# Kernel optimization log

Hardware: AMD Instinct MI355X
Metric: run time of the kernel (lower is better)

## Reference

```python
import jax, jax.numpy as jnp
import numpy as np

OCC_W, SMOOTH_W, SPARSE_W, CONS_W = 1.0, 0.1, 0.01, 0.1
EPS = 1e-7  # torch BCE clamps log terms; clip preds for numerical parity


def setup_inputs() -> dict:
    key = jax.random.key(0)
    k1, k2, k3, k4 = jax.random.split(key, 4)
    N, F = 16384, 64
    predictions = jax.random.uniform(k1, (N,), dtype=jnp.float32, minval=1e-4, maxval=1.0 - 1e-4)
    targets = jax.random.uniform(k2, (N,), dtype=jnp.float32)
    features = jax.random.normal(k3, (N, F), dtype=jnp.float32)
    points = jax.random.normal(k4, (N, 3), dtype=jnp.float32)
    return {"predictions": predictions, "targets": targets, "features": features, "points": points}


def reference(predictions, targets, features, points):
    # --- occupancy loss: BCE(mean) ---
    p = jnp.clip(predictions, EPS, 1.0 - EPS)
    occupancy = -jnp.mean(targets * jnp.log(p) + (1.0 - targets) * jnp.log1p(-p))

    # --- smoothness loss: for each point, 3 nearest neighbors (excl. self) ---
    # Fused all-pairs sq-distance [N, N] + top-k, replacing the per-point python loop.
    sq = jnp.sum(points * points, axis=1)                      # [N]
    d2 = sq[:, None] + sq[None, :] - 2.0 * (points @ points.T)  # [N, N]
    d2 = jnp.maximum(d2, 0.0)  # monotone in distance, so ordering == torch.norm ordering
    _, idx = jax.lax.top_k(-d2, 4)                              # 4 smallest distances
    nn_idx = idx[:, 1:4]                                        # drop self (index 0)
    # per-point local gradient: mean |pred_i - pred_nn|, then mean over points
    smoothness = jnp.mean(jnp.abs(predictions[:, None] - predictions[nn_idx]))

    # --- sparsity loss: mean |features| ---
    sparsity = jnp.mean(jnp.abs(features))

    # --- consistency loss: MSE ---
    consistency = jnp.mean((predictions - targets) ** 2)

    total = (OCC_W * occupancy + SMOOTH_W * smoothness
             + SPARSE_W * sparsity + CONS_W * consistency)
    return total
```

## Files before the change

### kernel.cpp

```cpp
#include <hip/hip_runtime.h>
#include <float.h>
#include <math.h>


constexpr int   N_ = 16384;
constexpr int   F_ = 64;
constexpr float OCC_W = 1.0f, SMOOTH_W = 0.1f, SPARSE_W = 0.01f, CONS_W = 0.1f;
constexpr float EPS_ = 1e-7f;

__device__ __forceinline__ void ins4f(float t, float& b0, float& b1, float& b2, float& b3) {
  float n0 = fminf(b0, t);
  float n1 = __builtin_amdgcn_fmed3f(b0, b1, t);
  float n2 = __builtin_amdgcn_fmed3f(b1, b2, t);
  float n3 = __builtin_amdgcn_fmed3f(b2, b3, t);
  b0 = n0; b1 = n1; b2 = n2; b3 = n3;
}


template <int CHUNKS>
__global__ __launch_bounds__(256) void knn_kernel(const float* __restrict__ pts,
                                                  float4* __restrict__ cand,
                                                  unsigned* __restrict__ done) {
  constexpr int CHUNK   = N_ / CHUNKS;
  constexpr int TILE    = CHUNK;
  constexpr int NOCT    = TILE / 8;
  constexpr int ITEMS   = 4;
  constexpr int IPG     = 1024;
  constexpr int IGROUPS = N_ / IPG;
  if (blockIdx.x == 0 && threadIdx.x == 0) *done = 0u;

  int igrp  = blockIdx.x % IGROUPS;
  int chunk = blockIdx.x / IGROUPS;
  int j0    = chunk * CHUNK;

  __shared__ float4 Q[TILE];
  for (int t = threadIdx.x; t < TILE; t += 256) {
    int j = j0 + t;
    float x = pts[3 * j], y = pts[3 * j + 1], z = pts[3 * j + 2];
    Q[t] = make_float4(-2.f * x, -2.f * y, -2.f * z, fmaf(x, x, fmaf(y, y, z * z)));
  }

  float xi[ITEMS], yi[ITEMS], zi[ITEMS];
  float b0[ITEMS], b1[ITEMS], b2[ITEMS], b3[ITEMS];
#pragma unroll
  for (int k = 0; k < ITEMS; ++k) {
    int i = igrp * IPG + threadIdx.x + k * 256;
    xi[k] = pts[3 * i]; yi[k] = pts[3 * i + 1]; zi[k] = pts[3 * i + 2];
    b0[k] = b1[k] = b2[k] = b3[k] = FLT_MAX;
  }
  __syncthreads();

  unsigned obase = (unsigned)(j0 >> 3);

  float4 c0 = Q[0], c1 = Q[1], c2 = Q[2], c3 = Q[3],
         c4 = Q[4], c5 = Q[5], c6 = Q[6], c7 = Q[7];
  for (int oct = 0; oct < NOCT; ++oct) {
    int nb = ((oct + 1) & (NOCT - 1)) * 8;
    float4 n0 = Q[nb + 0], n1 = Q[nb + 1], n2 = Q[nb + 2], n3 = Q[nb + 3],
           n4 = Q[nb + 4], n5 = Q[nb + 5], n6 = Q[nb + 6], n7 = Q[nb + 7];
    unsigned ok = obase + (unsigned)oct;
#pragma unroll
    for (int k = 0; k < ITEMS; ++k) {
      float x = xi[k], y = yi[k], z = zi[k];
      float t0 = fmaf(x, c0.x, fmaf(y, c0.y, fmaf(z, c0.z, c0.w)));
      float t1 = fmaf(x, c1.x, fmaf(y, c1.y, fmaf(z, c1.z, c1.w)));
      float t2 = fmaf(x, c2.x, fmaf(y, c2.y, fmaf(z, c2.z, c2.w)));
      float t3 = fmaf(x, c3.x, fmaf(y, c3.y, fmaf(z, c3.z, c3.w)));
      float t4 = fmaf(x, c4.x, fmaf(y, c4.y, fmaf(z, c4.z, c4.w)));
      float t5 = fmaf(x, c5.x, fmaf(y, c5.y, fmaf(z, c5.z, c5.w)));
      float t6 = fmaf(x, c6.x, fmaf(y, c6.y, fmaf(z, c6.z, c6.w)));
      float t7 = fmaf(x, c7.x, fmaf(y, c7.y, fmaf(z, c7.z, c7.w)));
      float m = fminf(fminf(fminf(t0, t1), fminf(t2, t3)),
                      fminf(fminf(t4, t5), fminf(t6, t7)));
      float kf = __uint_as_float((__float_as_uint(m) & 0xFFFFF000u) | ok);
      ins4f(kf, b0[k], b1[k], b2[k], b3[k]);
    }
    c0 = n0; c1 = n1; c2 = n2; c3 = n3; c4 = n4; c5 = n5; c6 = n6; c7 = n7;
  }

#pragma unroll
  for (int k = 0; k < ITEMS; ++k) {
    int i = igrp * IPG + threadIdx.x + k * 256;
    cand[(size_t)chunk * N_ + i] = make_float4(b0[k], b1[k], b2[k], b3[k]);
  }
}

template <int CHUNKS>
__global__ __launch_bounds__(256) void merge_kernel(const float* __restrict__ pred,
                                                    const float* __restrict__ targ,
                                                    const float* __restrict__ feat,
                                                    const float* __restrict__ pts,
                                                    const float4* __restrict__ cand,
                                                    float4* __restrict__ part,
                                                    unsigned* __restrict__ done,
                                                    float* __restrict__ out) {
  __shared__ float4 sh[256];
  __shared__ float ws4[4][4];
  __shared__ int is_last;
  constexpr int CPT = CHUNKS / 4;
  int tid  = threadIdx.x;
  int lane = tid & 63;
  int sub  = tid >> 6;
  int i = blockIdx.x * 64 + lane;

  const float4* f4 = (const float4*)feat;
  float s_sp = 0.f;
#pragma unroll
  for (int s = 0; s < 4; ++s) {
    float4 v = f4[(size_t)s * 65536 + blockIdx.x * 256 + tid];
    s_sp += fabsf(v.x) + fabsf(v.y) + fabsf(v.z) + fabsf(v.w);
  }

  float b0 = FLT_MAX, b1 = FLT_MAX, b2 = FLT_MAX, b3 = FLT_MAX;
#pragma unroll 4
  for (int cc = 0; cc < CPT; ++cc) {
    float4 v = cand[(size_t)(sub * CPT + cc) * N_ + i];
    ins4f(v.x, b0, b1, b2, b3);
    ins4f(v.y, b0, b1, b2, b3);
    ins4f(v.z, b0, b1, b2, b3);
    ins4f(v.w, b0, b1, b2, b3);
  }
  sh[tid] = make_float4(b0, b1, b2, b3);
  __syncthreads();

  float s_occ = 0.f, s_cons = 0.f, s_sm = 0.f;
  if (sub == 0) {
#pragma unroll
    for (int w = 1; w < 4; ++w) {
      float4 v = sh[w * 64 + lane];
      ins4f(v.x, b0, b1, b2, b3);
      ins4f(v.y, b0, b1, b2, b3);
      ins4f(v.z, b0, b1, b2, b3);
      ins4f(v.w, b0, b1, b2, b3);
    }
    unsigned qarr[4] = {__float_as_uint(b0) & 0xFFFu, __float_as_uint(b1) & 0xFFFu,
                        __float_as_uint(b2) & 0xFFFu, __float_as_uint(b3) & 0xFFFu};
    float xi = pts[3 * i], yi = pts[3 * i + 1], zi = pts[3 * i + 2];
    float c0 = FLT_MAX, c1 = FLT_MAX, c2 = FLT_MAX;
    float p0 = 0.f, p1 = 0.f, p2 = 0.f;
#pragma unroll
    for (int s = 0; s < 4; ++s) {
#pragma unroll
      for (int m = 0; m < 8; ++m) {
        int j = (int)(qarr[s] * 8 + m);
        float dx = xi - pts[3 * j], dy = yi - pts[3 * j + 1], dz = zi - pts[3 * j + 2];
        float d2 = fmaf(dx, dx, fmaf(dy, dy, dz * dz));
        float pj = pred[j];
        if (j != i && d2 < c2) {
          bool cc0 = d2 < c0, cc1 = d2 < c1;
          float n2 = cc1 ? c1 : d2;               float m2 = cc1 ? p1 : pj;
          float n1 = cc0 ? c0 : (cc1 ? d2 : c1);  float m1 = cc0 ? p0 : (cc1 ? pj : p1);
          float n0 = cc0 ? d2 : c0;               float m0 = cc0 ? pj : p0;
          c0 = n0; c1 = n1; c2 = n2; p0 = m0; p1 = m1; p2 = m2;
        }
      }
    }
    float pi = pred[i], tg = targ[i];
    float p  = fminf(fmaxf(pi, EPS_), 1.0f - EPS_);
    s_occ  = -(tg * __logf(p) + (1.0f - tg) * __logf(1.0f - p));
    float dd = pi - tg;
    s_cons = dd * dd;
    s_sm   = fabsf(pi - p0) + fabsf(pi - p1) + fabsf(pi - p2);
  }

  for (int off = 32; off > 0; off >>= 1) {
    s_sp   += __shfl_down(s_sp, off);
    s_occ  += __shfl_down(s_occ, off);
    s_cons += __shfl_down(s_cons, off);
    s_sm   += __shfl_down(s_sm, off);
  }
  if ((tid & 63) == 0) {
    int w = tid >> 6;
    ws4[w][0] = s_occ; ws4[w][1] = s_cons; ws4[w][2] = s_sp; ws4[w][3] = s_sm;
  }
  __syncthreads();
  if (tid == 0) {
    part[blockIdx.x] = make_float4(ws4[0][0] + ws4[1][0] + ws4[2][0] + ws4[3][0],
                                   ws4[0][1] + ws4[1][1] + ws4[2][1] + ws4[3][1],
                                   ws4[0][2] + ws4[1][2] + ws4[2][2] + ws4[3][2],
                                   ws4[0][3] + ws4[1][3] + ws4[2][3] + ws4[3][3]);
    __threadfence();
    unsigned prev = atomicAdd(done, 1u);
    is_last = (prev == (unsigned)(gridDim.x - 1));
  }
  __syncthreads();

  if (is_last) {
    __threadfence();
    float4 a = part[tid];
    float o = a.x, cn = a.y, sp = a.z, sm = a.w;
    for (int off = 32; off > 0; off >>= 1) {
      o  += __shfl_down(o, off);
      cn += __shfl_down(cn, off);
      sp += __shfl_down(sp, off);
      sm += __shfl_down(sm, off);
    }
    if ((tid & 63) == 0) {
      int w = tid >> 6;
      ws4[w][0] = o; ws4[w][1] = cn; ws4[w][2] = sp; ws4[w][3] = sm;
    }
    __syncthreads();
    if (tid == 0) {
      float occ  = ws4[0][0] + ws4[1][0] + ws4[2][0] + ws4[3][0];
      float cons = ws4[0][1] + ws4[1][1] + ws4[2][1] + ws4[3][1];
      float spar = ws4[0][2] + ws4[1][2] + ws4[2][2] + ws4[3][2];
      float smoo = ws4[0][3] + ws4[1][3] + ws4[2][3] + ws4[3][3];
      out[0] = OCC_W * (occ / (float)N_)
             + CONS_W * (cons / (float)N_)
             + SPARSE_W * (spar / (float)(N_ * F_))
             + SMOOTH_W * (smoo / (float)(N_ * 3));
    }
  }
}

extern "C" void kernel_launch(void* const* d_in, const int* in_sizes, int n_in,
                              void* d_out, int out_size, void* d_ws, size_t ws_size,
                              hipStream_t stream) {
  const float* pred = (const float*)d_in[0];
  const float* targ = (const float*)d_in[1];
  const float* feat = (const float*)d_in[2];
  const float* pts  = (const float*)d_in[3];
  float* out = (float*)d_out;

  char*     ws   = (char*)d_ws;
  float4*   part = (float4*)ws;
  unsigned* done = (unsigned*)(ws + 4096);
  float4*   cand = (float4*)(ws + 8192);

  size_t base = 8192;
  auto need = [&](int c) { return base + (size_t)c * N_ * 16; };
  if (ws_size >= need(64)) {
    knn_kernel<64><<<16 * 64, 256, 0, stream>>>(pts, cand, done);
    merge_kernel<64><<<256, 256, 0, stream>>>(pred, targ, feat, pts, cand, part, done, out);
  } else if (ws_size >= need(32)) {
    knn_kernel<32><<<16 * 32, 256, 0, stream>>>(pts, cand, done);
    merge_kernel<32><<<256, 256, 0, stream>>>(pred, targ, feat, pts, cand, part, done, out);
  } else {
    knn_kernel<16><<<16 * 16, 256, 0, stream>>>(pts, cand, done);
    merge_kernel<16><<<256, 256, 0, stream>>>(pred, targ, feat, pts, cand, part, done, out);
  }
}
```

Baseline: 110.5 us.

## Compute kNN distance tiles with bf16 split-precision MFMA instead of scalar FMAs

Replaces the scalar-FMA all-pairs distance kernel with a 32x32x16 bf16 MFMA kernel. Each fp32 coordinate is split into high and low bf16 halves so the dot product plus norm term is reconstructed at near-fp32 accuracy. Candidates are now tracked per group of 4 points instead of 8, which halves the exact rescoring work in the merge kernel. Chunking is fixed at 16 with 128-point i-blocks, removing the workspace-size dispatch. The hi/lo split drops the lo*lo cross terms, so near-tie neighbour ordering could differ slightly from exact fp32.

Measured after the change: 103.0 us. 1.07x faster.

```diff
diff --git a/kernel.cpp b/kernel.cpp
--- a/kernel.cpp
+++ b/kernel.cpp
@@ -7,6 +7,17 @@
 constexpr int   F_ = 64;
 constexpr float OCC_W = 1.0f, SMOOTH_W = 0.1f, SPARSE_W = 0.01f, CONS_W = 0.1f;
 constexpr float EPS_ = 1e-7f;
+
+constexpr int CHUNKS  = 16;
+constexpr int CHUNK_J = N_ / CHUNKS;
+constexpr int JTILES  = CHUNK_J / 32;
+constexpr int IB      = 128;
+constexpr int IBLOCKS = N_ / IB;
+
+typedef __attribute__((ext_vector_type(8)))  short bf16x8;
+typedef __attribute__((ext_vector_type(16))) float f32x16;
+
+union U128 { uint4 u; bf16x8 s; };
 
 __device__ __forceinline__ void ins4f(float t, float& b0, float& b1, float& b2, float& b3) {
   float n0 = fminf(b0, t);
@@ -16,76 +27,89 @@
   b0 = n0; b1 = n1; b2 = n2; b3 = n3;
 }
 
-
-template <int CHUNKS>
-__global__ __launch_bounds__(256) void knn_kernel(const float* __restrict__ pts,
-                                                  float4* __restrict__ cand,
-                                                  unsigned* __restrict__ done) {
-  constexpr int CHUNK   = N_ / CHUNKS;
-  constexpr int TILE    = CHUNK;
-  constexpr int NOCT    = TILE / 8;
-  constexpr int ITEMS   = 4;
-  constexpr int IPG     = 1024;
-  constexpr int IGROUPS = N_ / IPG;
+__device__ __forceinline__ void split2(float x, unsigned& h16, unsigned& l16) {
+  unsigned u = __float_as_uint(x);
+  unsigned r = u + 0x7FFFu + ((u >> 16) & 1u);
+  h16 = r >> 16;
+  float lo = x - __uint_as_float(r & 0xFFFF0000u);
+  unsigned v = __float_as_uint(lo);
+  l16 = (v + 0x7FFFu + ((v >> 16) & 1u)) >> 16;
+}
+
+
+__global__ __launch_bounds__(256) void knn_mfma(const float* __restrict__ pts,
+                                                float4* __restrict__ cand,
+                                                unsigned* __restrict__ done) {
   if (blockIdx.x == 0 && threadIdx.x == 0) *done = 0u;
-
-  int igrp  = blockIdx.x % IGROUPS;
-  int chunk = blockIdx.x / IGROUPS;
-  int j0    = chunk * CHUNK;
-
-  __shared__ float4 Q[TILE];
-  for (int t = threadIdx.x; t < TILE; t += 256) {
+  __shared__ uint4 AF[2][CHUNK_J];
+  const int tid   = threadIdx.x;
+  const int chunk = blockIdx.x & (CHUNKS - 1);
+  const int ibk   = blockIdx.x >> 4;
+  const int j0    = chunk * CHUNK_J;
+
+  for (int t = tid; t < CHUNK_J; t += 256) {
     int j = j0 + t;
-    float x = pts[3 * j], y = pts[3 * j + 1], z = pts[3 * j + 2];
-    Q[t] = make_float4(-2.f * x, -2.f * y, -2.f * z, fmaf(x, x, fmaf(y, y, z * z)));
-  }
-
-  float xi[ITEMS], yi[ITEMS], zi[ITEMS];
-  float b0[ITEMS], b1[ITEMS], b2[ITEMS], b3[ITEMS];
-#pragma unroll
-  for (int k = 0; k < ITEMS; ++k) {
-    int i = igrp * IPG + threadIdx.x + k * 256;
-    xi[k] = pts[3 * i]; yi[k] = pts[3 * i + 1]; zi[k] = pts[3 * i + 2];
-    b0[k] = b1[k] = b2[k] = b3[k] = FLT_MAX;
-  }
-  __syncthreads();
-
-  unsigned obase = (unsigned)(j0 >> 3);
-
-  float4 c0 = Q[0], c1 = Q[1], c2 = Q[2], c3 = Q[3],
-         c4 = Q[4], c5 = Q[5], c6 = Q[6], c7 = Q[7];
-  for (int oct = 0; oct < NOCT; ++oct) {
-    int nb = ((oct + 1) & (NOCT - 1)) * 8;
-    float4 n0 = Q[nb + 0], n1 = Q[nb + 1], n2 = Q[nb + 2], n3 = Q[nb + 3],
-           n4 = Q[nb + 4], n5 = Q[nb + 5], n6 = Q[nb + 6], n7 = Q[nb + 7];
-    unsigned ok = obase + (unsigned)oct;
-#pragma unroll
-    for (int k = 0; k < ITEMS; ++k) {
-      float x = xi[k], y = yi[k], z = zi[k];
-      float t0 = fmaf(x, c0.x, fmaf(y, c0.y, fmaf(z, c0.z, c0.w)));
-      float t1 = fmaf(x, c1.x, fmaf(y, c1.y, fmaf(z, c1.z, c1.w)));
-      float t2 = fmaf(x, c2.x, fmaf(y, c2.y, fmaf(z, c2.z, c2.w)));
-      float t3 = fmaf(x, c3.x, fmaf(y, c3.y, fmaf(z, c3.z, c3.w)));
-      float t4 = fmaf(x, c4.x, fmaf(y, c4.y, fmaf(z, c4.z, c4.w)));
-      float t5 = fmaf(x, c5.x, fmaf(y, c5.y, fmaf(z, c5.z, c5.w)));
-      float t6 = fmaf(x, c6.x, fmaf(y, c6.y, fmaf(z, c6.z, c6.w)));
-      float t7 = fmaf(x, c7.x, fmaf(y, c7.y, fmaf(z, c7.z, c7.w)));
-      float m = fminf(fminf(fminf(t0, t1), fminf(t2, t3)),
-                      fminf(fminf(t4, t5), fminf(t6, t7)));
-      float kf = __uint_as_float((__float_as_uint(m) & 0xFFFFF000u) | ok);
-      ins4f(kf, b0[k], b1[k], b2[k], b3[k]);
-    }
-    c0 = n0; c1 = n1; c2 = n2; c3 = n3; c4 = n4; c5 = n5; c6 = n6; c7 = n7;
-  }
-
-#pragma unroll
-  for (int k = 0; k < ITEMS; ++k) {
-    int i = igrp * IPG + threadIdx.x + k * 256;
-    cand[(size_t)chunk * N_ + i] = make_float4(b0[k], b1[k], b2[k], b3[k]);
-  }
-}
-
-template <int CHUNKS>
+    float qx = pts[3 * j], qy = pts[3 * j + 1], qz = pts[3 * j + 2];
+    float w  = fmaf(qx, qx, fmaf(qy, qy, qz * qz));
+    unsigned Hx, Lx, Hy, Ly, Hz, Lz, Hw, Lw;
+    split2(-2.f * qx, Hx, Lx);
+    split2(-2.f * qy, Hy, Ly);
+    split2(-2.f * qz, Hz, Lz);
+    split2(w, Hw, Lw);
+    AF[0][t] = make_uint4(Hx | (Hx << 16), Lx | (Lx << 16),
+                          Hy | (Hy << 16), Ly | (Ly << 16));
+    AF[1][t] = make_uint4(Hz | (Hz << 16), Lz | (Lz << 16),
+                          Hw | (Lw << 16), 0u);
+  }
+
+  const int lane = tid & 63, wv = tid >> 6;
+  const int h = lane >> 5, il = lane & 31;
+  const int i = ibk * IB + wv * 32 + il;
+  U128 bf;
+  {
+    float x = pts[3 * i], y = pts[3 * i + 1], z = pts[3 * i + 2];
+    unsigned hx, lx, hy, ly, hz, lz;
+    split2(x, hx, lx);
+    split2(y, hy, ly);
+    split2(z, hz, lz);
+    if (h == 0) {
+      unsigned a = hx | (lx << 16), b = hy | (ly << 16);
+      bf.u = make_uint4(a, a, b, b);
+    } else {
+      unsigned a = hz | (lz << 16);
+      bf.u = make_uint4(a, a, 0x3F803F80u, 0u);
+    }
+  }
+  __syncthreads();
+
+  float b0 = FLT_MAX, b1 = FLT_MAX, b2 = FLT_MAX, b3 = FLT_MAX;
+  const f32x16 zacc = {};
+  const unsigned qb0 = (unsigned)(chunk * 256 + h);
+  const uint4* __restrict__ afp = &AF[h][0];
+
+#pragma unroll 4
+  for (int t = 0; t < JTILES; ++t) {
+    U128 af; af.u = afp[t * 32 + il];
+    f32x16 acc = __builtin_amdgcn_mfma_f32_32x32x16_bf16(af.s, bf.s, zacc, 0, 0, 0);
+    unsigned q = qb0 + (unsigned)(t * 8);
+#pragma unroll
+    for (int g = 0; g < 4; ++g) {
+      float m = fminf(fminf(acc[4 * g + 0], acc[4 * g + 1]),
+                      fminf(acc[4 * g + 2], acc[4 * g + 3]));
+      float kf = __uint_as_float((__float_as_uint(m) & 0xFFFFF000u) | (q + 2u * g));
+      ins4f(kf, b0, b1, b2, b3);
+    }
+  }
+
+  float o0 = __shfl_xor(b0, 32), o1 = __shfl_xor(b1, 32),
+        o2 = __shfl_xor(b2, 32), o3 = __shfl_xor(b3, 32);
+  ins4f(o0, b0, b1, b2, b3);
+  ins4f(o1, b0, b1, b2, b3);
+  ins4f(o2, b0, b1, b2, b3);
+  ins4f(o3, b0, b1, b2, b3);
+  if (h == 0) cand[(size_t)chunk * N_ + i] = make_float4(b0, b1, b2, b3);
+}
+
 __global__ __launch_bounds__(256) void merge_kernel(const float* __restrict__ pred,
                                                     const float* __restrict__ targ,
                                                     const float* __restrict__ feat,
@@ -112,7 +136,7 @@
   }
 
   float b0 = FLT_MAX, b1 = FLT_MAX, b2 = FLT_MAX, b3 = FLT_MAX;
-#pragma unroll 4
+#pragma unroll
   for (int cc = 0; cc < CPT; ++cc) {
     float4 v = cand[(size_t)(sub * CPT + cc) * N_ + i];
     ins4f(v.x, b0, b1, b2, b3);
@@ -141,8 +165,8 @@
 #pragma unroll
     for (int s = 0; s < 4; ++s) {
 #pragma unroll
-      for (int m = 0; m < 8; ++m) {
-        int j = (int)(qarr[s] * 8 + m);
+      for (int m = 0; m < 4; ++m) {
+        int j = (int)(qarr[s] * 4 + m);
         float dx = xi - pts[3 * j], dy = yi - pts[3 * j + 1], dz = zi - pts[3 * j + 2];
         float d2 = fmaf(dx, dx, fmaf(dy, dy, dz * dz));
         float pj = pred[j];
@@ -227,16 +251,6 @@
   unsigned* done = (unsigned*)(ws + 4096);
   float4*   cand = (float4*)(ws + 8192);
 
-  size_t base = 8192;
-  auto need = [&](int c) { return base + (size_t)c * N_ * 16; };
-  if (ws_size >= need(64)) {
-    knn_kernel<64><<<16 * 64, 256, 0, stream>>>(pts, cand, done);
-    merge_kernel<64><<<256, 256, 0, stream>>>(pred, targ, feat, pts, cand, part, done, out);
-  } else if (ws_size >= need(32)) {
-    knn_kernel<32><<<16 * 32, 256, 0, stream>>>(pts, cand, done);
-    merge_kernel<32><<<256, 256, 0, stream>>>(pred, targ, feat, pts, cand, part, done, out);
-  } else {
-    knn_kernel<16><<<16 * 16, 256, 0, stream>>>(pts, cand, done);
-    merge_kernel<16><<<256, 256, 0, stream>>>(pred, targ, feat, pts, cand, part, done, out);
-  }
-}
+  knn_mfma<<<IBLOCKS * CHUNKS, 256, 0, stream>>>(pts, cand, done);
+  merge_kernel<<<256, 256, 0, stream>>>(pred, targ, feat, pts, cand, part, done, out);
+}
```
